# Kernel optimization log

Hardware: AMD Instinct MI355X
Metric: run time of the kernel (lower is better)

## Reference

```python
import jax, jax.numpy as jnp
import numpy as np
import math

N_NODES = 100000
N_EDGES = 1600000
D_FEAT = 32
K = 1        # Bernstein index k
N_ORD = 2    # Bernstein order n
COMB = float(math.comb(N_ORD, K))


def setup_inputs() -> dict:
    key = jax.random.key(0)
    k1, k2, k3 = jax.random.split(key, 3)
    feat = jax.random.normal(k1, (N_NODES, D_FEAT), dtype=jnp.float32)
    edge_src = jax.random.randint(k2, (N_EDGES,), 0, N_NODES)
    edge_dst = jax.random.randint(k3, (N_EDGES,), 0, N_NODES)
    return {"feat": feat, "edge_src": edge_src, "edge_dst": edge_dst}


def reference(feat, edge_src, edge_dst):
    # in-degree of each node (copy_u/sum aggregates over incoming edges)
    deg = jax.ops.segment_sum(jnp.ones((N_EDGES,), feat.dtype), edge_dst,
                              num_segments=N_NODES)
    d_invsqrt = jnp.clip(deg, 1.0, None) ** -0.5  # [N]
    d_invsqrt = d_invsqrt[:, None]                 # [N,1]

    def unn_laplacian(x):
        msg = (x * d_invsqrt)[edge_src]            # [E,D]
        agg = jax.ops.segment_sum(msg, edge_dst, num_segments=N_NODES)
        return x - agg * d_invsqrt

    if K == 0:
        h = feat
        for _ in range(N_ORD):
            h = unn_laplacian(h) / 2
            h = feat - h
    elif K == N_ORD:
        h = feat
        for _ in range(N_ORD):
            h = unn_laplacian(h) / 2
    else:
        temp = feat
        for _ in range(K):
            temp = unn_laplacian(temp) / 2
        h = feat
        for _ in range(N_ORD - K):
            h = unn_laplacian(h) / 2
            h = feat - h
        h = temp * h
    return COMB * h
```

## Files before the change

### kernel.cpp

```cpp
#include <hip/hip_runtime.h>

#define N_NODES 100000
#define N_EDGES 1600000
#define D_FEAT 32

#define BSH 7
#define BMASK 127
#define NB 782
#define CAPB 2432

#define P1_BS 512
#define P1_TILE 4096
#define P1_CAP 16


static __device__ __forceinline__ unsigned pack_bf16(float a, float b) {
    unsigned ua = __float_as_uint(a);
    unsigned ub = __float_as_uint(b);
    ua = (ua + 0x7FFFu + ((ua >> 16) & 1u)) >> 16;
    ub = (ub + 0x7FFFu + ((ub >> 16) & 1u)) >> 16;
    return (ua & 0xFFFFu) | (ub << 16);
}

__global__ void init_kernel(int* __restrict__ cursorA) {
    int b = blockIdx.x * blockDim.x + threadIdx.x;
    if (b < NB) cursorA[b] = b * CAPB;
}

__global__ void __launch_bounds__(P1_BS)
bucket_kernel(const int* __restrict__ edge_src,
              const int* __restrict__ edge_dst,
              int* __restrict__ cursorA,
              int* __restrict__ pairs, int n_edges) {
    __shared__ int s_cnt[NB];
    __shared__ int s_base[NB];
    __shared__ int s_off[NB + 1];
    __shared__ int s_buf[NB * P1_CAP];

    int tile = blockIdx.x * P1_TILE;
    if (tile >= n_edges) return;

    for (int b = threadIdx.x; b < NB; b += P1_BS) s_cnt[b] = 0;
    __syncthreads();

    const int4* src4 = reinterpret_cast<const int4*>(edge_src);
    const int4* dst4 = reinterpret_cast<const int4*>(edge_dst);
    int tileq = blockIdx.x * (P1_TILE / 4);
    #pragma unroll
    for (int j = 0; j < P1_TILE / 4 / P1_BS; ++j) {
        int iq = tileq + j * P1_BS + threadIdx.x;
        if (iq * 4 < n_edges) {
            int4 sv = src4[iq];
            int4 dv = dst4[iq];
            int ss[4] = {sv.x, sv.y, sv.z, sv.w};
            int dd[4] = {dv.x, dv.y, dv.z, dv.w};
            #pragma unroll
            for (int u = 0; u < 4; ++u) {
                int b = dd[u] >> BSH;
                int packed = (ss[u] << BSH) | (dd[u] & BMASK);
                int p = atomicAdd(&s_cnt[b], 1);
                if (p < P1_CAP) {
                    s_buf[b * P1_CAP + p] = packed;
                } else {
                    int gp = atomicAdd(&cursorA[b], 1);
                    pairs[gp] = packed;
                }
            }
        }
    }
    __syncthreads();

    for (int b = threadIdx.x; b < NB; b += P1_BS) {
        int c = min(s_cnt[b], P1_CAP);
        s_base[b] = atomicAdd(&cursorA[b], c);
        s_cnt[b] = c;
    }
    __syncthreads();
    if (threadIdx.x == 0) {
        int acc = 0;
        for (int b = 0; b < NB; ++b) { s_off[b] = acc; acc += s_cnt[b]; }
        s_off[NB] = acc;
    }
    __syncthreads();

    int total = s_off[NB];
    for (int t = threadIdx.x; t < total; t += P1_BS) {
        int lo = 0, hi = NB;
        while (hi - lo > 1) {
            int mid = (lo + hi) >> 1;
            if (t >= s_off[mid]) lo = mid; else hi = mid;
        }
        int idx = t - s_off[lo];
        pairs[s_base[lo] + idx] = s_buf[lo * P1_CAP + idx];
    }
}

__global__ void __launch_bounds__(256)
sort_kernel(const int* __restrict__ pairs,
            const int* __restrict__ cursorA,
            const float* __restrict__ feat,
            int* __restrict__ ssrc,
            int2* __restrict__ srange,
            float* __restrict__ dinv,
            unsigned* __restrict__ sfeat) {
    __shared__ int buf[CAPB];
    __shared__ int outb[CAPB];
    __shared__ int h[128];
    __shared__ int sc[128];
    __shared__ int cur[128];
    __shared__ float dv_s[128];

    int b = blockIdx.x;
    int t = threadIdx.x;
    int base = b * CAPB;
    int cnt = min(cursorA[b] - base, CAPB);

    if (t < 128) h[t] = 0;
    __syncthreads();
    for (int i = t; i < cnt; i += 256) {
        int p = pairs[base + i];
        buf[i] = p;
        atomicAdd(&h[p & BMASK], 1);
    }
    __syncthreads();

    int v = 0;
    if (t < 128) { v = h[t]; sc[t] = v; }
    __syncthreads();
    for (int off = 1; off < 128; off <<= 1) {
        int x = 0;
        if (t < 128 && t >= off) x = sc[t - off];
        __syncthreads();
        if (t < 128) sc[t] += x;
        __syncthreads();
    }
    if (t < 128) {
        int ex = sc[t] - v;
        cur[t] = ex;
        int node = (b << BSH) + t;
        if (node < N_NODES) {
            srange[node] = make_int2(base + ex, base + ex + v);
            float dvv = rsqrtf(fmaxf((float)v, 1.0f));
            dinv[node] = dvv;
            dv_s[t] = dvv;
        }
    }
    __syncthreads();

    for (int i = t; i < cnt; i += 256) {
        int p = buf[i];
        int pos = atomicAdd(&cur[p & BMASK], 1);
        outb[pos] = p >> BSH;
    }
    __syncthreads();
    for (int i = t; i < cnt; i += 256)
        ssrc[base + i] = outb[i];

    const float4* feat4 = reinterpret_cast<const float4*>(feat);
    uint4* sf4 = reinterpret_cast<uint4*>(sfeat);
    for (int idx = t; idx < 128 * 4; idx += 256) {
        int nl = idx >> 2;
        int q = idx & 3;
        int node = (b << BSH) + nl;
        if (node >= N_NODES) continue;
        float dvv = dv_s[nl];
        float4 fa = feat4[node * 8 + 2 * q];
        float4 fb = feat4[node * 8 + 2 * q + 1];
        uint4 pk;
        pk.x = pack_bf16(fa.x * dvv, fa.y * dvv);
        pk.y = pack_bf16(fa.z * dvv, fa.w * dvv);
        pk.z = pack_bf16(fb.x * dvv, fb.y * dvv);
        pk.w = pack_bf16(fb.z * dvv, fb.w * dvv);
        sf4[node * 4 + q] = pk;
    }
}

__global__ void gather_bf_kernel(const float* __restrict__ feat,
                                 const unsigned* __restrict__ sfeat,
                                 const int2* __restrict__ srange,
                                 const int* __restrict__ ssrc,
                                 const float* __restrict__ dinv,
                                 float* __restrict__ out) {
    int gid = blockIdx.x * blockDim.x + threadIdx.x;
    int node = gid >> 2;
    int q = gid & 3;
    if (node >= N_NODES) return;
    int2 se = srange[node];
    int k = se.x, en = se.y;
    const uint4* sf4 = reinterpret_cast<const uint4*>(sfeat);
    float a0 = 0.f, a1 = 0.f, a2 = 0.f, a3 = 0.f;
    float a4 = 0.f, a5 = 0.f, a6 = 0.f, a7 = 0.f;

    #define ACC(r)                                                 \
        a0 += __uint_as_float((r).x << 16);                        \
        a1 += __uint_as_float((r).x & 0xFFFF0000u);                \
        a2 += __uint_as_float((r).y << 16);                        \
        a3 += __uint_as_float((r).y & 0xFFFF0000u);                \
        a4 += __uint_as_float((r).z << 16);                        \
        a5 += __uint_as_float((r).z & 0xFFFF0000u);                \
        a6 += __uint_as_float((r).w << 16);                        \
        a7 += __uint_as_float((r).w & 0xFFFF0000u);

    for (; k + 3 < en; k += 4) {
        int s0 = ssrc[k],     s1 = ssrc[k + 1];
        int s2 = ssrc[k + 2], s3 = ssrc[k + 3];
        uint4 r0 = sf4[s0 * 4 + q];
        uint4 r1 = sf4[s1 * 4 + q];
        uint4 r2 = sf4[s2 * 4 + q];
        uint4 r3 = sf4[s3 * 4 + q];
        ACC(r0) ACC(r1) ACC(r2) ACC(r3)
    }
    for (; k < en; ++k) {
        uint4 r = sf4[ssrc[k] * 4 + q];
        ACC(r)
    }
    #undef ACC

    float dvn = dinv[node];
    const float4* feat4 = reinterpret_cast<const float4*>(feat);
    float4 fa = feat4[node * 8 + 2 * q];
    float4 fb = feat4[node * 8 + 2 * q + 1];
    float4 oa, ob;
    float y;
    y = 0.5f * (fa.x - a0 * dvn); oa.x = 2.0f * y * (fa.x - y);
    y = 0.5f * (fa.y - a1 * dvn); oa.y = 2.0f * y * (fa.y - y);
    y = 0.5f * (fa.z - a2 * dvn); oa.z = 2.0f * y * (fa.z - y);
    y = 0.5f * (fa.w - a3 * dvn); oa.w = 2.0f * y * (fa.w - y);
    y = 0.5f * (fb.x - a4 * dvn); ob.x = 2.0f * y * (fb.x - y);
    y = 0.5f * (fb.y - a5 * dvn); ob.y = 2.0f * y * (fb.y - y);
    y = 0.5f * (fb.z - a6 * dvn); ob.z = 2.0f * y * (fb.z - y);
    y = 0.5f * (fb.w - a7 * dvn); ob.w = 2.0f * y * (fb.w - y);
    float4* out4 = reinterpret_cast<float4*>(out);
    out4[node * 8 + 2 * q] = oa;
    out4[node * 8 + 2 * q + 1] = ob;
}

extern "C" void kernel_launch(void* const* d_in, const int* in_sizes, int n_in,
                              void* d_out, int out_size, void* d_ws, size_t ws_size,
                              hipStream_t stream) {
    const float* feat = (const float*)d_in[0];
    const int* edge_src = (const int*)d_in[1];
    const int* edge_dst = (const int*)d_in[2];
    float* out = (float*)d_out;

    int* ws = (int*)d_ws;
    int* cursorA   = ws;
    int2* srange   = (int2*)(cursorA + 1024);
    float* dinv    = (float*)(srange + N_NODES);
    int* ssrc      = (int*)(dinv + N_NODES);
    int* pairs     = ssrc + NB * CAPB;
    unsigned* sfeat = (unsigned*)(pairs + NB * CAPB);

    init_kernel<<<1, 1024, 0, stream>>>(cursorA);
    {
        int blocks = (N_EDGES + P1_TILE - 1) / P1_TILE;
        bucket_kernel<<<blocks, P1_BS, 0, stream>>>(edge_src, edge_dst,
                                                    cursorA, pairs, N_EDGES);
    }
    sort_kernel<<<NB, 256, 0, stream>>>(pairs, cursorA, feat, ssrc, srange,
                                        dinv, sfeat);
    {
        int total = N_NODES * 4;
        int blocks = (total + 255) / 256;
        gather_bf_kernel<<<blocks, 256, 0, stream>>>(feat, sfeat, srange,
                                                     ssrc, dinv, out);
    }
}
```

Before: 132.7 us.

## Simplify bucket flush, unroll gather by eight, use nontemporal feat/out access

```diff
diff --git a/kernel.cpp b/kernel.cpp
--- a/kernel.cpp
+++ b/kernel.cpp
@@ -13,6 +13,8 @@
 #define P1_TILE 4096
 #define P1_CAP 16
 
+
+typedef float v4f __attribute__((ext_vector_type(4)));
 
 static __device__ __forceinline__ unsigned pack_bf16(float a, float b) {
     unsigned ua = __float_as_uint(a);
@@ -34,7 +36,6 @@
               int* __restrict__ pairs, int n_edges) {
     __shared__ int s_cnt[NB];
     __shared__ int s_base[NB];
-    __shared__ int s_off[NB + 1];
     __shared__ int s_buf[NB * P1_CAP];
 
     int tile = blockIdx.x * P1_TILE;
@@ -72,26 +73,16 @@
 
     for (int b = threadIdx.x; b < NB; b += P1_BS) {
         int c = min(s_cnt[b], P1_CAP);
+        s_cnt[b] = c;
         s_base[b] = atomicAdd(&cursorA[b], c);
-        s_cnt[b] = c;
-    }
-    __syncthreads();
-    if (threadIdx.x == 0) {
-        int acc = 0;
-        for (int b = 0; b < NB; ++b) { s_off[b] = acc; acc += s_cnt[b]; }
-        s_off[NB] = acc;
-    }
-    __syncthreads();
-
-    int total = s_off[NB];
-    for (int t = threadIdx.x; t < total; t += P1_BS) {
-        int lo = 0, hi = NB;
-        while (hi - lo > 1) {
-            int mid = (lo + hi) >> 1;
-            if (t >= s_off[mid]) lo = mid; else hi = mid;
-        }
-        int idx = t - s_off[lo];
-        pairs[s_base[lo] + idx] = s_buf[lo * P1_CAP + idx];
+    }
+    __syncthreads();
+
+    for (int idx = threadIdx.x; idx < NB * P1_CAP; idx += P1_BS) {
+        int b = idx >> 4;
+        int slot = idx & (P1_CAP - 1);
+        if (slot < s_cnt[b])
+            pairs[s_base[b] + slot] = s_buf[idx];
     }
 }
 
@@ -201,6 +192,22 @@
         a6 += __uint_as_float((r).w << 16);                        \
         a7 += __uint_as_float((r).w & 0xFFFF0000u);
 
+    for (; k + 7 < en; k += 8) {
+        int s0 = ssrc[k],     s1 = ssrc[k + 1];
+        int s2 = ssrc[k + 2], s3 = ssrc[k + 3];
+        int s4 = ssrc[k + 4], s5 = ssrc[k + 5];
+        int s6 = ssrc[k + 6], s7 = ssrc[k + 7];
+        uint4 r0 = sf4[s0 * 4 + q];
+        uint4 r1 = sf4[s1 * 4 + q];
+        uint4 r2 = sf4[s2 * 4 + q];
+        uint4 r3 = sf4[s3 * 4 + q];
+        uint4 r4 = sf4[s4 * 4 + q];
+        uint4 r5 = sf4[s5 * 4 + q];
+        uint4 r6 = sf4[s6 * 4 + q];
+        uint4 r7 = sf4[s7 * 4 + q];
+        ACC(r0) ACC(r1) ACC(r2) ACC(r3)
+        ACC(r4) ACC(r5) ACC(r6) ACC(r7)
+    }
     for (; k + 3 < en; k += 4) {
         int s0 = ssrc[k],     s1 = ssrc[k + 1];
         int s2 = ssrc[k + 2], s3 = ssrc[k + 3];
@@ -217,10 +224,10 @@
     #undef ACC
 
     float dvn = dinv[node];
-    const float4* feat4 = reinterpret_cast<const float4*>(feat);
-    float4 fa = feat4[node * 8 + 2 * q];
-    float4 fb = feat4[node * 8 + 2 * q + 1];
-    float4 oa, ob;
+    const v4f* featv = reinterpret_cast<const v4f*>(feat);
+    v4f fa = __builtin_nontemporal_load(&featv[node * 8 + 2 * q]);
+    v4f fb = __builtin_nontemporal_load(&featv[node * 8 + 2 * q + 1]);
+    v4f oa, ob;
     float y;
     y = 0.5f * (fa.x - a0 * dvn); oa.x = 2.0f * y * (fa.x - y);
     y = 0.5f * (fa.y - a1 * dvn); oa.y = 2.0f * y * (fa.y - y);
@@ -230,9 +237,9 @@
     y = 0.5f * (fb.y - a5 * dvn); ob.y = 2.0f * y * (fb.y - y);
     y = 0.5f * (fb.z - a6 * dvn); ob.z = 2.0f * y * (fb.z - y);
     y = 0.5f * (fb.w - a7 * dvn); ob.w = 2.0f * y * (fb.w - y);
-    float4* out4 = reinterpret_cast<float4*>(out);
-    out4[node * 8 + 2 * q] = oa;
-    out4[node * 8 + 2 * q + 1] = ob;
+    v4f* outv = reinterpret_cast<v4f*>(out);
+    __builtin_nontemporal_store(oa, &outv[node * 8 + 2 * q]);
+    __builtin_nontemporal_store(ob, &outv[node * 8 + 2 * q + 1]);
 }
 
 extern "C" void kernel_launch(void* const* d_in, const int* in_sizes, int n_in,
```

Measured after the change: 119.9 us. -9.7%, faster.
